# Kernel tuning notes

Hardware: AMD Instinct MI355X
Metric: run time of the kernel (lower is better)

Reference implementation:

```python
import jax, jax.numpy as jnp
import numpy as np

N_NODES = 50000
N_EDGES = 800000
IN_FEATS = 256
H_FEATS = 256
NUM_CLASSES = 128


def setup_inputs() -> dict:
    key = jax.random.key(0)
    ks = jax.random.split(key, 5)
    x = jax.random.normal(ks[0], (N_NODES, IN_FEATS), dtype=jnp.float32)
    src = jax.random.randint(ks[1], (N_EDGES,), 0, N_NODES, dtype=jnp.int64)
    dst = jax.random.randint(ks[2], (N_EDGES,), 0, N_NODES, dtype=jnp.int64)
    W1 = jax.random.normal(ks[3], (IN_FEATS, H_FEATS), dtype=jnp.float32) * (1.0 / np.sqrt(IN_FEATS))
    b1 = jnp.zeros((H_FEATS,), dtype=jnp.float32)
    W2 = jax.random.normal(ks[4], (H_FEATS, NUM_CLASSES), dtype=jnp.float32) * (1.0 / np.sqrt(H_FEATS))
    b2 = jnp.zeros((NUM_CLASSES,), dtype=jnp.float32)
    return {"x": x, "src": src, "dst": dst, "W1": W1, "b1": b1, "W2": W2, "b2": b2}


def _graph_conv(x, src, dst, norm_src, norm_dst, W, b):
    # DGL GraphConv, norm='both': D_out^{-1/2} A D_in^{-1/2} X W + b
    # project first (in_feats >= out_feats -> cheaper messages), math identical
    h = (x * norm_src[:, None]) @ W                      # [N, out]
    agg = jax.ops.segment_sum(h[src], dst, num_segments=N_NODES)  # gather + scatter-add
    return agg * norm_dst[:, None] + b


def reference(x, src, dst, W1, b1, W2, b2):
    ones = jnp.ones((N_EDGES,), dtype=x.dtype)
    deg_out = jax.ops.segment_sum(ones, src, num_segments=N_NODES)
    deg_in = jax.ops.segment_sum(ones, dst, num_segments=N_NODES)
    norm_src = jnp.clip(deg_out, 1.0, None) ** -0.5
    norm_dst = jnp.clip(deg_in, 1.0, None) ** -0.5

    h = _graph_conv(x, src, dst, norm_src, norm_dst, W1, b1)
    h = jax.nn.relu(h)
    out = _graph_conv(h, src, dst, norm_src, norm_dst, W2, b2)
    return out
```

## Files before the change

### kernel.cpp

```cpp
#include <hip/hip_runtime.h>

#define NNODES 50000
#define MPAD   50048
#define NEDGES 800000
#define KDIM   256
#define FH     256
#define FOUT   128

#define SHIFT  8
#define NBUCK  196
#define NB1    200
#define EPB    4000

typedef __bf16 bf16x8 __attribute__((ext_vector_type(8)));
typedef float floatx4 __attribute__((ext_vector_type(4)));

__device__ __forceinline__ float bf2f(unsigned short u) {
    union { unsigned int i; float f; } v;
    v.i = ((unsigned int)u) << 16;
    return v.f;
}
__device__ __forceinline__ unsigned short f2bf(float f) {
    union { float f; unsigned int i; } v;
    v.f = f;
    unsigned int r = v.i + 0x7FFFu + ((v.i >> 16) & 1u);
    return (unsigned short)(r >> 16);
}

__global__ __launch_bounds__(256) void l1_sort_cast(const int* __restrict__ src,
                                                    const int* __restrict__ dst,
                                                    unsigned int* __restrict__ tmp1,
                                                    unsigned char* __restrict__ tmp2,
                                                    int* __restrict__ exD_arr,
                                                    int* __restrict__ exS_arr,
                                                    const float* __restrict__ W1,
                                                    unsigned short* __restrict__ Wt1,
                                                    const float* __restrict__ W2,
                                                    unsigned short* __restrict__ Wt2) {
    __shared__ int histD[256], histS[256], exD[256], exS[256];
    __shared__ unsigned int bufD[EPB];
    __shared__ unsigned short bufS[EPB];
    __shared__ float tile[32][33];
    const int tid = threadIdx.x;

    if (blockIdx.x >= NB1) {
        int b = blockIdx.x - NB1;
        const float* W; unsigned short* Wt; int N;
        if (b < 64) { W = W1; Wt = Wt1; N = FH; }
        else        { b -= 64; W = W2; Wt = Wt2; N = FOUT; }
        int kt = (b & 7) * 32;
        int nt = (b >> 3) * 32;
        int tx = tid & 31;
        int ty = tid >> 5;
        for (int r = ty; r < 32; r += 8)
            tile[r][tx] = W[(size_t)(kt + r) * N + nt + tx];
        __syncthreads();
        for (int r = ty; r < 32; r += 8)
            Wt[(size_t)(nt + r) * KDIM + kt + tx] = f2bf(tile[tx][r]);
        return;
    }

    const int b = blockIdx.x;
    const int base = b * EPB;
    histD[tid] = 0; histS[tid] = 0;
    __syncthreads();
    for (int g = tid; g < EPB / 4; g += 256) {
        uint4 s4 = *(const uint4*)(src + base + g * 4);
        uint4 d4 = *(const uint4*)(dst + base + g * 4);
        atomicAdd(&histD[d4.x >> SHIFT], 1);
        atomicAdd(&histD[d4.y >> SHIFT], 1);
        atomicAdd(&histD[d4.z >> SHIFT], 1);
        atomicAdd(&histD[d4.w >> SHIFT], 1);
        atomicAdd(&histS[s4.x >> SHIFT], 1);
        atomicAdd(&histS[s4.y >> SHIFT], 1);
        atomicAdd(&histS[s4.z >> SHIFT], 1);
        atomicAdd(&histS[s4.w >> SHIFT], 1);
    }
    __syncthreads();
    int vD = histD[tid], vS = histS[tid];
    exD[tid] = vD; exS[tid] = vS;
    __syncthreads();
    for (int off = 1; off < 256; off <<= 1) {
        int tD = (tid >= off) ? exD[tid - off] : 0;
        int tS = (tid >= off) ? exS[tid - off] : 0;
        __syncthreads();
        exD[tid] += tD; exS[tid] += tS;
        __syncthreads();
    }
    int eD = exD[tid] - vD, eS = exS[tid] - vS;
    exD_arr[tid * NB1 + b] = eD;
    exS_arr[tid * NB1 + b] = eS;
    __syncthreads();
    histD[tid] = eD; histS[tid] = eS;
    __syncthreads();
    for (int g = tid; g < EPB / 4; g += 256) {
        uint4 s4 = *(const uint4*)(src + base + g * 4);
        uint4 d4 = *(const uint4*)(dst + base + g * 4);
        unsigned int ss[4] = {s4.x, s4.y, s4.z, s4.w};
        unsigned int dd[4] = {d4.x, d4.y, d4.z, d4.w};
#pragma unroll
        for (int j = 0; j < 4; ++j) {
            int p = atomicAdd(&histD[dd[j] >> SHIFT], 1);
            bufD[p] = (ss[j] << 16) | dd[j];
            int q = atomicAdd(&histS[ss[j] >> SHIFT], 1);
            bufS[q] = (unsigned short)ss[j];
        }
    }
    __syncthreads();
    for (int e = tid; e < EPB; e += 256) tmp1[base + e] = bufD[e];
    for (int e = tid; e < EPB; e += 256) tmp2[base + e] = (unsigned char)(bufS[e] & 255u);
}

__global__ __launch_bounds__(256) void l2_both(const unsigned int* __restrict__ tmp1,
                                               const unsigned char* __restrict__ tmp2,
                                               const int* __restrict__ exD_arr,
                                               const int* __restrict__ exS_arr,
                                               int* __restrict__ row_ptr,
                                               float* __restrict__ norm_dst,
                                               float* __restrict__ norm_src,
                                               int* __restrict__ csr_src) {
    __shared__ int cnt[256], ofs[256], cur[256], red[256];
    __shared__ int segoff[NB1], seglen[NB1];
    const int tid = threadIdx.x;

    if (blockIdx.x >= NBUCK) {
        const int k = blockIdx.x - NBUCK;
        if (tid < NB1) {
            int e0 = exS_arr[k * NB1 + tid];
            segoff[tid] = tid * EPB + e0;
            seglen[tid] = exS_arr[(k + 1) * NB1 + tid] - e0;
        }
        cnt[tid] = 0;
        __syncthreads();
        if (tid < NB1) {
            int so = segoff[tid], sl = seglen[tid];
            for (int i = 0; i < sl; ++i)
                atomicAdd(&cnt[tmp2[so + i]], 1);
        }
        __syncthreads();
        int node = k * 256 + tid;
        if (node < NNODES) {
            int d = cnt[tid] < 1 ? 1 : cnt[tid];
            norm_src[node] = 1.0f / sqrtf((float)d);
        }
        return;
    }

    const int k = blockIdx.x;
    int e0v = 0;
    if (tid < NB1) {
        e0v = exD_arr[k * NB1 + tid];
        segoff[tid] = tid * EPB + e0v;
        seglen[tid] = exD_arr[(k + 1) * NB1 + tid] - e0v;
    }
    red[tid] = (tid < NB1) ? e0v : 0;
    cnt[tid] = 0;
    __syncthreads();
    for (int off = 128; off > 0; off >>= 1) {
        if (tid < off) red[tid] += red[tid + off];
        __syncthreads();
    }
    const int base = red[0];
    if (tid < NB1) {
        int so = segoff[tid], sl = seglen[tid];
        for (int i = 0; i < sl; ++i)
            atomicAdd(&cnt[tmp1[so + i] & 255u], 1);
    }
    __syncthreads();
    int v = cnt[tid];
    ofs[tid] = v;
    __syncthreads();
    for (int off = 1; off < 256; off <<= 1) {
        int t = (tid >= off) ? ofs[tid - off] : 0;
        __syncthreads();
        ofs[tid] += t;
        __syncthreads();
    }
    int excl = ofs[tid] - v;
    int node = k * 256 + tid;
    if (node < NNODES) {
        row_ptr[node] = base + excl;
        int d = v < 1 ? 1 : v;
        norm_dst[node] = 1.0f / sqrtf((float)d);
    }
    cur[tid] = base + excl;
    if (k == 0 && tid == 0) row_ptr[NNODES] = NEDGES;
    __syncthreads();
    if (tid < NB1) {
        int so = segoff[tid], sl = seglen[tid];
        for (int i = 0; i < sl; ++i) {
            unsigned int p = tmp1[so + i];
            int pos = atomicAdd(&cur[p & 255u], 1);
            csr_src[pos] = (int)(p >> 16);
        }
    }
}

struct arawF { float4 v[8]; float sc; };
struct arawU { uint4 v[4]; };
template <typename TA> struct rawsel;
template <> struct rawsel<float> { using type = arawF; };
template <> struct rawsel<unsigned short> { using type = arawU; };

__device__ __forceinline__ void loadA_raw(const float* A, const float* norm,
                                          int mt, int arow, int akseg, arawF& r) {
    int row = mt * 64 + arow;
    if (row < NNODES) {
        const float* p = A + (size_t)row * KDIM + akseg;
#pragma unroll
        for (int j = 0; j < 8; ++j) r.v[j] = *(const float4*)(p + j * 4);
        r.sc = norm[row];
    } else {
        float4 z = {0.f, 0.f, 0.f, 0.f};
#pragma unroll
        for (int j = 0; j < 8; ++j) r.v[j] = z;
        r.sc = 0.f;
    }
}
__device__ __forceinline__ void loadA_raw(const unsigned short* A, const float*,
                                          int mt, int arow, int akseg, arawU& r) {
    const unsigned short* p = A + (size_t)(mt * 64 + arow) * KDIM + akseg;
#pragma unroll
    for (int j = 0; j < 4; ++j) r.v[j] = *(const uint4*)(p + j * 8);
}
__device__ __forceinline__ void writeA_lds(char* Asb, int arow, int akseg, const arawF& r) {
    const int s = (arow & 7) << 4;
    const int base = arow * 512;
#pragma unroll
    for (int j = 0; j < 4; ++j) {
        union { uint4 u; unsigned short h[8]; } o;
        float4 a = r.v[2 * j], b = r.v[2 * j + 1];
        o.h[0] = f2bf(a.x * r.sc); o.h[1] = f2bf(a.y * r.sc);
        o.h[2] = f2bf(a.z * r.sc); o.h[3] = f2bf(a.w * r.sc);
        o.h[4] = f2bf(b.x * r.sc); o.h[5] = f2bf(b.y * r.sc);
        o.h[6] = f2bf(b.z * r.sc); o.h[7] = f2bf(b.w * r.sc);
        *(uint4*)(Asb + base + (((akseg + j * 8) * 2) ^ s)) = o.u;
    }
}
__device__ __forceinline__ void writeA_lds(char* Asb, int arow, int akseg, const arawU& r) {
    const int s = (arow & 7) << 4;
    const int base = arow * 512;
#pragma unroll
    for (int j = 0; j < 4; ++j)
        *(uint4*)(Asb + base + (((akseg + j * 8) * 2) ^ s)) = r.v[j];
}

template <typename TA, bool SCALE, int NPANEL>
__global__ __launch_bounds__(512) void gemm_bres(const TA* __restrict__ A,
                                                 const unsigned short* __restrict__ Bt,
                                                 const float* __restrict__ norm,
                                                 unsigned short* __restrict__ C) {
    constexpr int N = 128 * NPANEL;
    constexpr int NTILES = MPAD / 64;
    __shared__ __align__(16) unsigned short Bs[128 * 256];
    __shared__ __align__(16) unsigned short As[64 * 256];
    char* Bsb = (char*)Bs;
    char* Asb = (char*)As;

    const int tid = threadIdx.x;
    const int lane = tid & 63;
    const int wave = tid >> 6;

    int col0, mt0, mstep;
    if (NPANEL == 2) {
        col0 = ((blockIdx.x >> 3) & 1) * 128;
        mt0 = ((blockIdx.x >> 4) << 3) + (blockIdx.x & 7);
        mstep = gridDim.x >> 1;
    } else {
        col0 = 0;
        mt0 = blockIdx.x;
        mstep = gridDim.x;
    }

    {
        int col = tid >> 2;
        int kq = (tid & 3) * 64;
        const unsigned short* bg = Bt + (size_t)(col0 + col) * KDIM + kq;
        const int s = (col & 7) << 4;
        const int base = col * 512;
#pragma unroll
        for (int j = 0; j < 8; ++j) {
            uint4 v = *(const uint4*)(bg + j * 8);
            *(uint4*)(Bsb + base + (((kq + j * 8) * 2) ^ s)) = v;
        }
    }

    const int arow = tid >> 3;
    const int akseg = (tid & 7) * 32;

    typename rawsel<TA>::type buf;
    loadA_raw(A, norm, mt0, arow, akseg, buf);
    writeA_lds(Asb, arow, akseg, buf);
    __syncthreads();
    int mt = mt0, mtn = mt0 + mstep;
    if (mtn < NTILES) loadA_raw(A, norm, mtn, arow, akseg, buf);

    const int wn = wave & 3, wm = wave >> 2;
    const int ar = lane & 15;
    const int fkb = (lane >> 4) << 4;
    const int rA0 = wm * 32 + ar,  rA1 = rA0 + 16;
    const int cB0 = wn * 32 + ar,  cB1 = cB0 + 16;
    const int aO0 = rA0 * 512, aS0 = (rA0 & 7) << 4;
    const int aO1 = rA1 * 512, aS1 = (rA1 & 7) << 4;
    const int bO0 = cB0 * 512, bS0 = (cB0 & 7) << 4;
    const int bO1 = cB1 * 512, bS1 = (cB1 & 7) << 4;
    const int rb = (lane >> 4) << 2, cc = lane & 15;

    for (;;) {
        floatx4 a00 = {}, a01 = {}, a10 = {}, a11 = {};
#pragma unroll
        for (int kk = 0; kk < 8; ++kk) {
            const int kb = kk * 64 + fkb;
            bf16x8 fa0 = *(const bf16x8*)(Asb + aO0 + (kb ^ aS0));
            bf16x8 fa1 = *(const bf16x8*)(Asb + aO1 + (kb ^ aS1));
            bf16x8 fb0 = *(const bf16x8*)(Bsb + bO0 + (kb ^ bS0));
            bf16x8 fb1 = *(const bf16x8*)(Bsb + bO1 + (kb ^ bS1));
            a00 = __builtin_amdgcn_mfma_f32_16x16x32_bf16(fa0, fb0, a00, 0, 0, 0);
            a01 = __builtin_amdgcn_mfma_f32_16x16x32_bf16(fa0, fb1, a01, 0, 0, 0);
            a10 = __builtin_amdgcn_mfma_f32_16x16x32_bf16(fa1, fb0, a10, 0, 0, 0);
            a11 = __builtin_amdgcn_mfma_f32_16x16x32_bf16(fa1, fb1, a11, 0, 0, 0);
        }
        {
            const int mBase = mt * 64 + wm * 32 + rb;
            const int cBase = col0 + wn * 32 + cc;
#pragma unroll
            for (int r = 0; r < 4; ++r) {
                int m = mBase + r;
                C[(size_t)m * N + cBase]      = f2bf(a00[r]);
                C[(size_t)m * N + cBase + 16] = f2bf(a01[r]);
                int m2 = m + 16;
                C[(size_t)m2 * N + cBase]      = f2bf(a10[r]);
                C[(size_t)m2 * N + cBase + 16] = f2bf(a11[r]);
            }
        }
        if (mtn >= NTILES) break;
        __syncthreads();
        writeA_lds(Asb, arow, akseg, buf);
        mt = mtn; mtn += mstep;
        __syncthreads();
        if (mtn < NTILES) loadA_raw(A, norm, mtn, arow, akseg, buf);
    }
}

__global__ __launch_bounds__(256) void agg1_kernel(const unsigned short* __restrict__ H,
                                                   const int* __restrict__ row_ptr,
                                                   const int* __restrict__ csr_src,
                                                   const float* __restrict__ norm_dst,
                                                   const float* __restrict__ norm_src,
                                                   const float* __restrict__ bias,
                                                   unsigned short* __restrict__ out) {
    const int F = 256;
    const int tid = threadIdx.x;
    const int lane = tid & 63;
    const int half = lane >> 5;
    const int f0 = (lane & 31) * 8;
    const int nA = __builtin_amdgcn_readfirstlane(blockIdx.x * 8 + (tid >> 6) * 2);
    const int node = nA + half;

    const int rp0 = row_ptr[nA < NNODES ? nA : NNODES];
    const int rp1 = row_ptr[nA + 1 < NNODES ? nA + 1 : NNODES];
    const int rp2 = row_ptr[nA + 2 < NNODES ? nA + 2 : NNODES];
    const int degA = rp1 - rp0, degB = rp2 - rp1;
    const int nIter = degA > degB ? degA : degB;

    const unsigned short* Hl = H + f0;
    float acc[8] = {};

    for (int it = 0; it < nIter; it += 4) {
        int ix[4];
#pragma unroll
        for (int u = 0; u < 4; ++u) {
            int iA = csr_src[rp0 + it + u];
            int iB = csr_src[rp1 + it + u];
            iA = (it + u < degA) ? iA : NNODES;
            iB = (it + u < degB) ? iB : NNODES;
            ix[u] = half ? iB : iA;
        }
        uint4 v[4];
#pragma unroll
        for (int u = 0; u < 4; ++u)
            v[u] = *(const uint4*)(Hl + (size_t)ix[u] * F);
#pragma unroll
        for (int u = 0; u < 4; ++u) {
            const unsigned short* pv = (const unsigned short*)&v[u];
#pragma unroll
            for (int j = 0; j < 8; ++j) acc[j] += bf2f(pv[j]);
        }
    }

    float nd = 0.f, ns = 0.f;
    if (node < NNODES) { nd = norm_dst[node]; ns = norm_src[node]; }
    float4 b0 = *(const float4*)(bias + f0);
    float4 b1v = *(const float4*)(bias + f0 + 4);
    float bb[8] = {b0.x, b0.y, b0.z, b0.w, b1v.x, b1v.y, b1v.z, b1v.w};
    union { uint4 u; unsigned short s[8]; } o;
#pragma unroll
    for (int j = 0; j < 8; ++j)
        o.s[j] = f2bf(fmaxf(fmaf(acc[j], nd, bb[j]), 0.f) * ns);
    *(uint4*)(out + (size_t)node * F + f0) = o.u;
}

__global__ __launch_bounds__(256) void agg2_kernel(const unsigned short* __restrict__ H,
                                                   const int* __restrict__ row_ptr,
                                                   const int* __restrict__ csr_src,
                                                   const float* __restrict__ norm_dst,
                                                   const float* __restrict__ bias,
                                                   float* __restrict__ out) {
    const int F = 128;
    const int tid = threadIdx.x;
    const int lane = tid & 63;
    const int q = lane >> 4;
    const int f0 = (lane & 15) * 8;
    const int n0 = __builtin_amdgcn_readfirstlane(blockIdx.x * 16 + (tid >> 6) * 4);
    const int node = n0 + q;

    int rp[5];
#pragma unroll
    for (int j = 0; j < 5; ++j) rp[j] = row_ptr[(n0 + j) < NNODES ? (n0 + j) : NNODES];
    int dg[4];
    int nIter = 0;
#pragma unroll
    for (int j = 0; j < 4; ++j) { dg[j] = rp[j + 1] - rp[j]; nIter = dg[j] > nIter ? dg[j] : nIter; }

    const unsigned short* Hl = H + f0;
    float acc[8] = {};

    for (int it = 0; it < nIter; it += 4) {
        int ix[4];
#pragma unroll
        for (int u = 0; u < 4; ++u) {
            int i0 = csr_src[rp[0] + it + u];
            int i1 = csr_src[rp[1] + it + u];
            int i2 = csr_src[rp[2] + it + u];
            int i3 = csr_src[rp[3] + it + u];
            i0 = (it + u < dg[0]) ? i0 : NNODES;
            i1 = (it + u < dg[1]) ? i1 : NNODES;
            i2 = (it + u < dg[2]) ? i2 : NNODES;
            i3 = (it + u < dg[3]) ? i3 : NNODES;
            int ilo = (q & 1) ? i1 : i0;
            int ihi = (q & 1) ? i3 : i2;
            ix[u] = (q & 2) ? ihi : ilo;
        }
        uint4 v[4];
#pragma unroll
        for (int u = 0; u < 4; ++u)
            v[u] = *(const uint4*)(Hl + (size_t)ix[u] * F);
#pragma unroll
        for (int u = 0; u < 4; ++u) {
            const unsigned short* pv = (const unsigned short*)&v[u];
#pragma unroll
            for (int j = 0; j < 8; ++j) acc[j] += bf2f(pv[j]);
        }
    }

    if (node < NNODES) {
        float nd = norm_dst[node];
        float4 o1, o2;
        o1.x = fmaf(acc[0], nd, bias[f0 + 0]);
        o1.y = fmaf(acc[1], nd, bias[f0 + 1]);
        o1.z = fmaf(acc[2], nd, bias[f0 + 2]);
        o1.w = fmaf(acc[3], nd, bias[f0 + 3]);
        o2.x = fmaf(acc[4], nd, bias[f0 + 4]);
        o2.y = fmaf(acc[5], nd, bias[f0 + 5]);
        o2.z = fmaf(acc[6], nd, bias[f0 + 6]);
        o2.w = fmaf(acc[7], nd, bias[f0 + 7]);
        *(float4*)(out + (size_t)node * F + f0) = o1;
        *(float4*)(out + (size_t)node * F + f0 + 4) = o2;
    }
}

extern "C" void kernel_launch(void* const* d_in, const int* in_sizes, int n_in,
                              void* d_out, int out_size, void* d_ws, size_t ws_size,
                              hipStream_t stream) {
    const float* x   = (const float*)d_in[0];
    const int*   src = (const int*)d_in[1];
    const int*   dst = (const int*)d_in[2];
    const float* W1  = (const float*)d_in[3];
    const float* b1  = (const float*)d_in[4];
    const float* W2  = (const float*)d_in[5];
    const float* b2  = (const float*)d_in[6];
    float* out = (float*)d_out;

    char* ws = (char*)d_ws;
    size_t off = 0;
    auto alloc = [&](size_t bytes) {
        char* p = ws + off;
        off += (bytes + 255) & ~(size_t)255;
        return p;
    };
    float* norm_src  = (float*)alloc(NNODES * 4);
    float* norm_dst  = (float*)alloc(NNODES * 4);
    int*   exD_arr   = (int*)alloc((size_t)256 * NB1 * 4);
    int*   exS_arr   = (int*)alloc((size_t)256 * NB1 * 4);
    unsigned int*  tmp1 = (unsigned int*)alloc((size_t)NEDGES * 4);
    unsigned char* tmp2 = (unsigned char*)alloc((size_t)NEDGES);
    int*   row_ptr   = (int*)alloc((NNODES + 16) * 4);
    int*   csr_src   = (int*)alloc((size_t)(NEDGES + 256) * 4);
    unsigned short* h   = (unsigned short*)alloc((size_t)MPAD * FH * 2);
    unsigned short* h1  = (unsigned short*)alloc((size_t)MPAD * FH * 2);
    unsigned short* Wt1 = (unsigned short*)alloc((size_t)FH * KDIM * 2);
    unsigned short* Wt2 = (unsigned short*)alloc((size_t)FOUT * KDIM * 2);
    unsigned short* h2  = h;

    l1_sort_cast<<<NB1 + 96, 256, 0, stream>>>(src, dst, tmp1, tmp2, exD_arr, exS_arr,
                                               W1, Wt1, W2, Wt2);
    l2_both<<<2 * NBUCK, 256, 0, stream>>>(tmp1, tmp2, exD_arr, exS_arr,
                                           row_ptr, norm_dst, norm_src, csr_src);

    gemm_bres<float, true, 2><<<512, 512, 0, stream>>>(x, Wt1, norm_src, h);
    agg1_kernel<<<MPAD / 8, 256, 0, stream>>>(h, row_ptr, csr_src, norm_dst, norm_src, b1, h1);

    gemm_bres<unsigned short, false, 1><<<256, 512, 0, stream>>>(h1, Wt2, nullptr, h2);
    agg2_kernel<<<(NNODES + 15) / 16, 256, 0, stream>>>(h2, row_ptr, csr_src, norm_dst, b2, out);
}
```

Baseline: 252.7 us.

## Store intermediate features in 32-column chunked layout for cache-friendly gathers

```diff
diff --git a/kernel.cpp b/kernel.cpp
--- a/kernel.cpp
+++ b/kernel.cpp
@@ -6,6 +6,7 @@
 #define KDIM   256
 #define FH     256
 #define FOUT   128
+#define FCH    32
 
 #define SHIFT  8
 #define NBUCK  196
@@ -219,7 +220,7 @@
 }
 __device__ __forceinline__ void loadA_raw(const unsigned short* A, const float*,
                                           int mt, int arow, int akseg, arawU& r) {
-    const unsigned short* p = A + (size_t)(mt * 64 + arow) * KDIM + akseg;
+    const unsigned short* p = A + ((size_t)(akseg >> 5) * MPAD + mt * 64 + arow) * FCH;
 #pragma unroll
     for (int j = 0; j < 4; ++j) r.v[j] = *(const uint4*)(p + j * 8);
 }
@@ -250,7 +251,6 @@
                                                  const unsigned short* __restrict__ Bt,
                                                  const float* __restrict__ norm,
                                                  unsigned short* __restrict__ C) {
-    constexpr int N = 128 * NPANEL;
     constexpr int NTILES = MPAD / 64;
     __shared__ __align__(16) unsigned short Bs[128 * 256];
     __shared__ __align__(16) unsigned short As[64 * 256];
@@ -306,6 +306,8 @@
     const int bO1 = cB1 * 512, bS1 = (cB1 & 7) << 4;
     const int rb = (lane >> 4) << 2, cc = lane & 15;
 
+    unsigned short* Cb = C + ((size_t)((col0 >> 5) + wn) * MPAD) * FCH;
+
     for (;;) {
         floatx4 a00 = {}, a01 = {}, a10 = {}, a11 = {};
 #pragma unroll
@@ -322,15 +324,14 @@
         }
         {
             const int mBase = mt * 64 + wm * 32 + rb;
-            const int cBase = col0 + wn * 32 + cc;
 #pragma unroll
             for (int r = 0; r < 4; ++r) {
                 int m = mBase + r;
-                C[(size_t)m * N + cBase]      = f2bf(a00[r]);
-                C[(size_t)m * N + cBase + 16] = f2bf(a01[r]);
+                Cb[(size_t)m * FCH + cc]      = f2bf(a00[r]);
+                Cb[(size_t)m * FCH + cc + 16] = f2bf(a01[r]);
                 int m2 = m + 16;
-                C[(size_t)m2 * N + cBase]      = f2bf(a10[r]);
-                C[(size_t)m2 * N + cBase + 16] = f2bf(a11[r]);
+                Cb[(size_t)m2 * FCH + cc]      = f2bf(a10[r]);
+                Cb[(size_t)m2 * FCH + cc + 16] = f2bf(a11[r]);
             }
         }
         if (mtn >= NTILES) break;
@@ -349,55 +350,49 @@
                                                    const float* __restrict__ norm_src,
                                                    const float* __restrict__ bias,
                                                    unsigned short* __restrict__ out) {
-    const int F = 256;
+    const int c = blockIdx.x & 7;
+    const int nb = blockIdx.x >> 3;
     const int tid = threadIdx.x;
     const int lane = tid & 63;
-    const int half = lane >> 5;
-    const int f0 = (lane & 31) * 8;
-    const int nA = __builtin_amdgcn_readfirstlane(blockIdx.x * 8 + (tid >> 6) * 2);
-    const int node = nA + half;
-
-    const int rp0 = row_ptr[nA < NNODES ? nA : NNODES];
-    const int rp1 = row_ptr[nA + 1 < NNODES ? nA + 1 : NNODES];
-    const int rp2 = row_ptr[nA + 2 < NNODES ? nA + 2 : NNODES];
-    const int degA = rp1 - rp0, degB = rp2 - rp1;
-    const int nIter = degA > degB ? degA : degB;
-
-    const unsigned short* Hl = H + f0;
+    const int g = lane >> 2;
+    const int f0 = (lane & 3) * 8;
+    const int node = nb * 64 + (tid >> 6) * 16 + g;
+
+    const unsigned short* Hc = H + ((size_t)c * MPAD) * FCH + f0;
     float acc[8] = {};
 
-    for (int it = 0; it < nIter; it += 4) {
-        int ix[4];
-#pragma unroll
-        for (int u = 0; u < 4; ++u) {
-            int iA = csr_src[rp0 + it + u];
-            int iB = csr_src[rp1 + it + u];
-            iA = (it + u < degA) ? iA : NNODES;
-            iB = (it + u < degB) ? iB : NNODES;
-            ix[u] = half ? iB : iA;
-        }
-        uint4 v[4];
-#pragma unroll
-        for (int u = 0; u < 4; ++u)
-            v[u] = *(const uint4*)(Hl + (size_t)ix[u] * F);
-#pragma unroll
-        for (int u = 0; u < 4; ++u) {
-            const unsigned short* pv = (const unsigned short*)&v[u];
-#pragma unroll
-            for (int j = 0; j < 8; ++j) acc[j] += bf2f(pv[j]);
-        }
+    int e0 = 0, e1 = 0;
+    if (node < NNODES) { e0 = row_ptr[node]; e1 = row_ptr[node + 1]; }
+
+    for (int e = e0; e < e1; e += 4) {
+        int i0 = csr_src[e];
+        int i1 = csr_src[e + 1];
+        int i2 = csr_src[e + 2];
+        int i3 = csr_src[e + 3];
+        i1 = (e + 1 < e1) ? i1 : NNODES;
+        i2 = (e + 2 < e1) ? i2 : NNODES;
+        i3 = (e + 3 < e1) ? i3 : NNODES;
+        uint4 v0 = *(const uint4*)(Hc + (size_t)i0 * FCH);
+        uint4 v1 = *(const uint4*)(Hc + (size_t)i1 * FCH);
+        uint4 v2 = *(const uint4*)(Hc + (size_t)i2 * FCH);
+        uint4 v3 = *(const uint4*)(Hc + (size_t)i3 * FCH);
+        const unsigned short* p0 = (const unsigned short*)&v0;
+        const unsigned short* p1 = (const unsigned short*)&v1;
+        const unsigned short* p2 = (const unsigned short*)&v2;
+        const unsigned short* p3 = (const unsigned short*)&v3;
+#pragma unroll
+        for (int j = 0; j < 8; ++j)
+            acc[j] += bf2f(p0[j]) + bf2f(p1[j]) + bf2f(p2[j]) + bf2f(p3[j]);
     }
 
     float nd = 0.f, ns = 0.f;
     if (node < NNODES) { nd = norm_dst[node]; ns = norm_src[node]; }
-    float4 b0 = *(const float4*)(bias + f0);
-    float4 b1v = *(const float4*)(bias + f0 + 4);
-    float bb[8] = {b0.x, b0.y, b0.z, b0.w, b1v.x, b1v.y, b1v.z, b1v.w};
+    const int fg = c * FCH + f0;
     union { uint4 u; unsigned short s[8]; } o;
 #pragma unroll
     for (int j = 0; j < 8; ++j)
-        o.s[j] = f2bf(fmaxf(fmaf(acc[j], nd, bb[j]), 0.f) * ns);
-    *(uint4*)(out + (size_t)node * F + f0) = o.u;
+        o.s[j] = f2bf(fmaxf(fmaf(acc[j], nd, bias[fg + j]), 0.f) * ns);
+    *(uint4*)(out + ((size_t)c * MPAD + node) * FCH + f0) = o.u;
 }
 
 __global__ __launch_bounds__(256) void agg2_kernel(const unsigned short* __restrict__ H,
@@ -406,67 +401,55 @@
                                                    const float* __restrict__ norm_dst,
                                                    const float* __restrict__ bias,
                                                    float* __restrict__ out) {
-    const int F = 128;
+    const int c = (blockIdx.x & 7) >> 1;
+    const int nb = (blockIdx.x >> 3) * 2 + (blockIdx.x & 1);
     const int tid = threadIdx.x;
     const int lane = tid & 63;
-    const int q = lane >> 4;
-    const int f0 = (lane & 15) * 8;
-    const int n0 = __builtin_amdgcn_readfirstlane(blockIdx.x * 16 + (tid >> 6) * 4);
-    const int node = n0 + q;
-
-    int rp[5];
-#pragma unroll
-    for (int j = 0; j < 5; ++j) rp[j] = row_ptr[(n0 + j) < NNODES ? (n0 + j) : NNODES];
-    int dg[4];
-    int nIter = 0;
-#pragma unroll
-    for (int j = 0; j < 4; ++j) { dg[j] = rp[j + 1] - rp[j]; nIter = dg[j] > nIter ? dg[j] : nIter; }
-
-    const unsigned short* Hl = H + f0;
+    const int g = lane >> 2;
+    const int f0 = (lane & 3) * 8;
+    const int node = nb * 64 + (tid >> 6) * 16 + g;
+    if (node >= NNODES) return;
+
+    const unsigned short* Hc = H + ((size_t)c * MPAD) * FCH + f0;
     float acc[8] = {};
 
-    for (int it = 0; it < nIter; it += 4) {
-        int ix[4];
-#pragma unroll
-        for (int u = 0; u < 4; ++u) {
-            int i0 = csr_src[rp[0] + it + u];
-            int i1 = csr_src[rp[1] + it + u];
-            int i2 = csr_src[rp[2] + it + u];
-            int i3 = csr_src[rp[3] + it + u];
-            i0 = (it + u < dg[0]) ? i0 : NNODES;
-            i1 = (it + u < dg[1]) ? i1 : NNODES;
-            i2 = (it + u < dg[2]) ? i2 : NNODES;
-            i3 = (it + u < dg[3]) ? i3 : NNODES;
-            int ilo = (q & 1) ? i1 : i0;
-            int ihi = (q & 1) ? i3 : i2;
-            ix[u] = (q & 2) ? ihi : ilo;
-        }
-        uint4 v[4];
-#pragma unroll
-        for (int u = 0; u < 4; ++u)
-            v[u] = *(const uint4*)(Hl + (size_t)ix[u] * F);
-#pragma unroll
-        for (int u = 0; u < 4; ++u) {
-            const unsigned short* pv = (const unsigned short*)&v[u];
-#pragma unroll
-            for (int j = 0; j < 8; ++j) acc[j] += bf2f(pv[j]);
-        }
-    }
-
-    if (node < NNODES) {
-        float nd = norm_dst[node];
-        float4 o1, o2;
-        o1.x = fmaf(acc[0], nd, bias[f0 + 0]);
-        o1.y = fmaf(acc[1], nd, bias[f0 + 1]);
-        o1.z = fmaf(acc[2], nd, bias[f0 + 2]);
-        o1.w = fmaf(acc[3], nd, bias[f0 + 3]);
-        o2.x = fmaf(acc[4], nd, bias[f0 + 4]);
-        o2.y = fmaf(acc[5], nd, bias[f0 + 5]);
-        o2.z = fmaf(acc[6], nd, bias[f0 + 6]);
-        o2.w = fmaf(acc[7], nd, bias[f0 + 7]);
-        *(float4*)(out + (size_t)node * F + f0) = o1;
-        *(float4*)(out + (size_t)node * F + f0 + 4) = o2;
-    }
+    int e0 = row_ptr[node];
+    int e1 = row_ptr[node + 1];
+
+    for (int e = e0; e < e1; e += 4) {
+        int i0 = csr_src[e];
+        int i1 = csr_src[e + 1];
+        int i2 = csr_src[e + 2];
+        int i3 = csr_src[e + 3];
+        i1 = (e + 1 < e1) ? i1 : NNODES;
+        i2 = (e + 2 < e1) ? i2 : NNODES;
+        i3 = (e + 3 < e1) ? i3 : NNODES;
+        uint4 v0 = *(const uint4*)(Hc + (size_t)i0 * FCH);
+        uint4 v1 = *(const uint4*)(Hc + (size_t)i1 * FCH);
+        uint4 v2 = *(const uint4*)(Hc + (size_t)i2 * FCH);
+        uint4 v3 = *(const uint4*)(Hc + (size_t)i3 * FCH);
+        const unsigned short* p0 = (const unsigned short*)&v0;
+        const unsigned short* p1 = (const unsigned short*)&v1;
+        const unsigned short* p2 = (const unsigned short*)&v2;
+        const unsigned short* p3 = (const unsigned short*)&v3;
+#pragma unroll
+        for (int j = 0; j < 8; ++j)
+            acc[j] += bf2f(p0[j]) + bf2f(p1[j]) + bf2f(p2[j]) + bf2f(p3[j]);
+    }
+
+    float nd = norm_dst[node];
+    const int fg = c * FCH + f0;
+    float4 o1, o2;
+    o1.x = fmaf(acc[0], nd, bias[fg + 0]);
+    o1.y = fmaf(acc[1], nd, bias[fg + 1]);
+    o1.z = fmaf(acc[2], nd, bias[fg + 2]);
+    o1.w = fmaf(acc[3], nd, bias[fg + 3]);
+    o2.x = fmaf(acc[4], nd, bias[fg + 4]);
+    o2.y = fmaf(acc[5], nd, bias[fg + 5]);
+    o2.z = fmaf(acc[6], nd, bias[fg + 6]);
+    o2.w = fmaf(acc[7], nd, bias[fg + 7]);
+    *(float4*)(out + (size_t)node * FOUT + fg) = o1;
+    *(float4*)(out + (size_t)node * FOUT + fg + 4) = o2;
 }
 
 extern "C" void kernel_launch(void* const* d_in, const int* in_sizes, int n_in,
@@ -508,8 +491,8 @@
                                            row_ptr, norm_dst, norm_src, csr_src);
 
     gemm_bres<float, true, 2><<<512, 512, 0, stream>>>(x, Wt1, norm_src, h);
-    agg1_kernel<<<MPAD / 8, 256, 0, stream>>>(h, row_ptr, csr_src, norm_dst, norm_src, b1, h1);
+    agg1_kernel<<<(MPAD / 64) * 8, 256, 0, stream>>>(h, row_ptr, csr_src, norm_dst, norm_src, b1, h1);
 
     gemm_bres<unsigned short, false, 1><<<256, 512, 0, stream>>>(h1, Wt2, nullptr, h2);
-    agg2_kernel<<<(NNODES + 15) / 16, 256, 0, stream>>>(h2, row_ptr, csr_src, norm_dst, b2, out);
-}
+    agg2_kernel<<<((MPAD / 64 + 1) / 2) * 8, 256, 0, stream>>>(h2, row_ptr, csr_src, norm_dst, b2, out);
+}
```

After: 254.1 us. About the same (+0.5%).
